# Kernel optimization log

Hardware: AMD Instinct MI355X
Metric: run time of the kernel (lower is better)

The kernel has to match this reference:

```python
import jax, jax.numpy as jnp
import numpy as np

N_NODES = 20000
N_EDGES = 640000
HIDDEN = 256
HEADS = 8
HEAD_DIM = HIDDEN // HEADS
VOCAB = 119
N_FEATS = 9


def setup_inputs() -> dict:
    key = jax.random.key(0)
    ks = jax.random.split(key, 12)
    X = jax.random.randint(ks[0], (N_NODES, N_FEATS), 0, VOCAB)
    edge_row = jnp.sort(jax.random.randint(ks[1], (N_EDGES,), 0, N_NODES))
    edge_col = jax.random.randint(ks[2], (N_EDGES,), 0, N_NODES)
    s = 0.05  # init scale to keep activations sane
    emb_tables = jax.random.normal(ks[3], (N_FEATS, VOCAB, HIDDEN), jnp.float32) * s
    q_w = jax.random.normal(ks[4], (HIDDEN, HIDDEN), jnp.float32) * s
    q_b = jax.random.normal(ks[5], (HIDDEN,), jnp.float32) * s
    k_w = jax.random.normal(ks[6], (HIDDEN, HIDDEN), jnp.float32) * s
    k_b = jax.random.normal(ks[7], (HIDDEN,), jnp.float32) * s
    v_w = jax.random.normal(ks[8], (HIDDEN, HIDDEN), jnp.float32) * s
    v_b = jax.random.normal(ks[9], (HIDDEN,), jnp.float32) * s
    o_w = jax.random.normal(ks[10], (HIDDEN, HIDDEN), jnp.float32) * s
    o_b = jax.random.normal(ks[11], (HIDDEN,), jnp.float32) * s
    return dict(X=X, edge_row=edge_row, edge_col=edge_col, emb_tables=emb_tables,
                q_w=q_w, q_b=q_b, k_w=k_w, k_b=k_b, v_w=v_w, v_b=v_b, o_w=o_w, o_b=o_b)


def reference(X, edge_row, edge_col, emb_tables, q_w, q_b, k_w, k_b, v_w, v_b, o_w, o_b):
    N = X.shape[0]
    # AtomEncoder: sum of per-feature embeddings -> [N, HIDDEN]
    feat_idx = jnp.arange(N_FEATS)[None, :]  # [1, 9]
    h = emb_tables[feat_idx, X].sum(axis=1)  # [N, 9, H] -> [N, H]
    # q/k/v projections (torch Linear: y = x W^T + b), split into heads
    q = (h @ q_w.T + q_b).reshape(N, HEADS, HEAD_DIM) * (HEAD_DIM ** -0.5)
    k = (h @ k_w.T + k_b).reshape(N, HEADS, HEAD_DIM)
    v = (h @ v_w.T + v_b).reshape(N, HEADS, HEAD_DIM)
    # SDDMM: per-edge, per-head scores
    s = jnp.einsum('ehd,ehd->eh', q[edge_row], k[edge_col])  # [E, HEADS]
    # sparse row-wise softmax (over each node's outgoing-edge neighbors)
    m = jax.ops.segment_max(s, edge_row, num_segments=N)
    e = jnp.exp(s - m[edge_row])
    z = jax.ops.segment_sum(e, edge_row, num_segments=N)
    attn = e / z[edge_row]  # [E, HEADS]
    # SPMM: weighted aggregation of neighbor values
    out = jax.ops.segment_sum(attn[:, :, None] * v[edge_col], edge_row, num_segments=N)
    return out.reshape(N, HIDDEN) @ o_w.T + o_b
```

## Files before the change

kernel.cpp:

```cpp
#include <hip/hip_runtime.h>
#include <hip/hip_bf16.h>

#define N_NODES 20000
#define N_EDGES 640000
#define HIDDEN 256
#define HEADS 8
#define HEAD_DIM 32
#define N_FEATS 9
#define VOCAB 119

typedef __hip_bfloat16 bf16;
typedef __attribute__((ext_vector_type(8))) short short8;
typedef __attribute__((ext_vector_type(4))) float f32x4;

__device__ __forceinline__ ushort f2u(float x) { union { ushort u; bf16 b; } c; c.b = __float2bfloat16(x); return c.u; }
__device__ __forceinline__ void unpack8(uint4 u, float* f) {
    f[0] = __uint_as_float(u.x << 16); f[1] = __uint_as_float(u.x & 0xffff0000u);
    f[2] = __uint_as_float(u.y << 16); f[3] = __uint_as_float(u.y & 0xffff0000u);
    f[4] = __uint_as_float(u.z << 16); f[5] = __uint_as_float(u.z & 0xffff0000u);
    f[6] = __uint_as_float(u.w << 16); f[7] = __uint_as_float(u.w & 0xffff0000u);
}
__device__ __forceinline__ uint pack2(float a, float b) {
    union { __hip_bfloat162 h; uint u; } c;
    c.h = __float22bfloat162_rn(make_float2(a, b));
    return c.u;
}

#if __has_builtin(__builtin_amdgcn_fdot2_f32_bf16)
typedef __attribute__((ext_vector_type(2))) __bf16 bf16x2_t;
__device__ __forceinline__ float dot2bf(uint a, uint b, float c) {
    return __builtin_amdgcn_fdot2_f32_bf16(__builtin_bit_cast(bf16x2_t, a),
                                           __builtin_bit_cast(bf16x2_t, b), c, false);
}
#else
__device__ __forceinline__ float dot2bf(uint a, uint b, float c) {
    return c + __uint_as_float(a << 16) * __uint_as_float(b << 16)
             + __uint_as_float(a & 0xffff0000u) * __uint_as_float(b & 0xffff0000u);
}
#endif

__global__ void k_pre(const int* __restrict__ X, const float* __restrict__ emb,
                      bf16* __restrict__ h,
                      const float* __restrict__ qw, const float* __restrict__ kw,
                      const float* __restrict__ vw, const float* __restrict__ ow,
                      const float* __restrict__ qb, const float* __restrict__ kb,
                      const float* __restrict__ vb,
                      bf16* __restrict__ wqkv, bf16* __restrict__ wo,
                      float* __restrict__ qkvb,
                      const int* __restrict__ erow, int* __restrict__ row_ptr) {
    int b = blockIdx.x;
    if (b < 5000) {
        int tid = b * 256 + threadIdx.x;
        int n = tid >> 6;
        int c4 = (tid & 63) * 4;
        float4 a = make_float4(0.f, 0.f, 0.f, 0.f);
#pragma unroll
        for (int f = 0; f < N_FEATS; ++f) {
            int idx = X[n * N_FEATS + f];
            float4 e = *(const float4*)(emb + ((size_t)(f * VOCAB + idx)) * HIDDEN + c4);
            a.x += e.x; a.y += e.y; a.z += e.z; a.w += e.w;
        }
        ushort4 o = make_ushort4(f2u(a.x), f2u(a.y), f2u(a.z), f2u(a.w));
        *(ushort4*)((ushort*)h + (size_t)n * HIDDEN + c4) = o;
    } else if (b < 6027) {
        int i = (b - 5000) * 256 + threadIdx.x;
        if (i < 196608) {
            const float* s = i < 65536 ? qw : i < 131072 ? kw : vw;
            wqkv[i] = __float2bfloat16(s[i & 65535]);
        } else if (i < 262144) {
            wo[i - 196608] = __float2bfloat16(ow[i - 196608]);
        } else if (i < 262912) {
            int j = i - 262144;
            const float* s = j < 256 ? qb : j < 512 ? kb : vb;
            qkvb[j] = s[j & 255];
        }
    } else {
        int n = (b - 6027) * 256 + threadIdx.x;
        if (n > N_NODES) return;
        int lo = 0, hi = N_EDGES;
        while (lo < hi) {
            int mid = (lo + hi) >> 1;
            if (erow[mid] < n) lo = mid + 1; else hi = mid;
        }
        row_ptr[n] = lo;
    }
}

template <int MODE, bool GUARD, int TM>
__device__ __forceinline__ void gemm_core(const bf16* __restrict__ A,
                                          const bf16* __restrict__ W,
                                          const float* __restrict__ bias,
                                          void* __restrict__ Y0, void* __restrict__ Y1,
                                          float s_q, int n0, int d0) {
    constexpr int RI = TM / 32;
    __shared__ short As[TM * 72];
    __shared__ short Bs[128 * 72];
    int t = threadIdx.x;
    int lane = t & 63, w = t >> 6;
    int wr = (w >> 1) * (TM / 2), wc = (w & 1) * 64;
    int lr = lane & 15, quad = lane >> 4;

    f32x4 acc[RI][4] = {};
    short8 ra[RI], rb[4];
    int srowA[RI], skoA[RI], srowB[4], skoB[4];
#pragma unroll
    for (int it = 0; it < RI; ++it) { int c = t + 256 * it; srowA[it] = c >> 3; skoA[it] = (c & 7) * 8; }
#pragma unroll
    for (int it = 0; it < 4; ++it) { int c = t + 256 * it; srowB[it] = c >> 3; skoB[it] = (c & 7) * 8; }

#pragma unroll
    for (int it = 0; it < RI; ++it) {
        int n = n0 + srowA[it];
        short8 av = {};
        if (!GUARD || n < N_NODES) av = *(const short8*)(A + (size_t)n * HIDDEN + skoA[it]);
        ra[it] = av;
    }
#pragma unroll
    for (int it = 0; it < 4; ++it)
        rb[it] = *(const short8*)(W + (size_t)(d0 + srowB[it]) * HIDDEN + skoB[it]);
#pragma unroll
    for (int it = 0; it < RI; ++it) *(short8*)(&As[srowA[it] * 72 + skoA[it]]) = ra[it];
#pragma unroll
    for (int it = 0; it < 4; ++it)  *(short8*)(&Bs[srowB[it] * 72 + skoB[it]]) = rb[it];
    __syncthreads();

    for (int k0 = 64; k0 < 256; k0 += 64) {
#pragma unroll
        for (int it = 0; it < RI; ++it) {
            int n = n0 + srowA[it];
            short8 av = {};
            if (!GUARD || n < N_NODES) av = *(const short8*)(A + (size_t)n * HIDDEN + k0 + skoA[it]);
            ra[it] = av;
        }
#pragma unroll
        for (int it = 0; it < 4; ++it)
            rb[it] = *(const short8*)(W + (size_t)(d0 + srowB[it]) * HIDDEN + k0 + skoB[it]);
        {
            short8 af[RI][2], bfr[4][2];
#pragma unroll
            for (int i = 0; i < RI; ++i)
#pragma unroll
                for (int kk = 0; kk < 2; ++kk)
                    af[i][kk] = *(short8*)(&As[(wr + i * 16 + lr) * 72 + kk * 32 + quad * 8]);
#pragma unroll
            for (int j = 0; j < 4; ++j)
#pragma unroll
                for (int kk = 0; kk < 2; ++kk)
                    bfr[j][kk] = *(short8*)(&Bs[(wc + j * 16 + lr) * 72 + kk * 32 + quad * 8]);
#pragma unroll
            for (int kk = 0; kk < 2; ++kk)
#pragma unroll
                for (int i = 0; i < RI; ++i)
#pragma unroll
                    for (int j = 0; j < 4; ++j)
                        acc[i][j] = __builtin_amdgcn_mfma_f32_16x16x32_bf16(
                            af[i][kk], bfr[j][kk], acc[i][j], 0, 0, 0);
        }
        __syncthreads();
#pragma unroll
        for (int it = 0; it < RI; ++it) *(short8*)(&As[srowA[it] * 72 + skoA[it]]) = ra[it];
#pragma unroll
        for (int it = 0; it < 4; ++it)  *(short8*)(&Bs[srowB[it] * 72 + skoB[it]]) = rb[it];
        __syncthreads();
    }
    {
        short8 af[RI][2], bfr[4][2];
#pragma unroll
        for (int i = 0; i < RI; ++i)
#pragma unroll
            for (int kk = 0; kk < 2; ++kk)
                af[i][kk] = *(short8*)(&As[(wr + i * 16 + lr) * 72 + kk * 32 + quad * 8]);
#pragma unroll
        for (int j = 0; j < 4; ++j)
#pragma unroll
            for (int kk = 0; kk < 2; ++kk)
                bfr[j][kk] = *(short8*)(&Bs[(wc + j * 16 + lr) * 72 + kk * 32 + quad * 8]);
#pragma unroll
        for (int kk = 0; kk < 2; ++kk)
#pragma unroll
            for (int i = 0; i < RI; ++i)
#pragma unroll
                for (int j = 0; j < 4; ++j)
                    acc[i][j] = __builtin_amdgcn_mfma_f32_16x16x32_bf16(
                        af[i][kk], bfr[j][kk], acc[i][j], 0, 0, 0);
    }

#pragma unroll
    for (int j = 0; j < 4; ++j) {
        int dbase = d0 + wc + j * 16;
        float bj = bias[dbase + lr];
        if constexpr (MODE == 0) {
            float sc = (dbase < 256) ? s_q : 1.f;
            ushort* dst; int stride;
            if (dbase < 256) {
                dst = (ushort*)Y0 + (size_t)(dbase >> 6) * N_NODES * 64 + (dbase & 63) + lr;
                stride = 64;
            } else if (dbase < 512) {
                int e = dbase - 256;
                dst = (ushort*)Y1 + (size_t)(e >> 6) * N_NODES * 128 + (e & 63) + lr;
                stride = 128;
            } else {
                int e = dbase - 512;
                dst = (ushort*)Y1 + (size_t)(e >> 6) * N_NODES * 128 + 64 + (e & 63) + lr;
                stride = 128;
            }
#pragma unroll
            for (int i = 0; i < RI; ++i)
#pragma unroll
                for (int r = 0; r < 4; ++r) {
                    int n = n0 + wr + i * 16 + quad * 4 + r;
                    if (GUARD && n >= N_NODES) continue;
                    dst[(size_t)n * stride] = f2u((acc[i][j][r] + bj) * sc);
                }
        } else {
            float* dst = (float*)Y0 + dbase + lr;
#pragma unroll
            for (int i = 0; i < RI; ++i)
#pragma unroll
                for (int r = 0; r < 4; ++r) {
                    int n = n0 + wr + i * 16 + quad * 4 + r;
                    if (GUARD && n >= N_NODES) continue;
                    dst[(size_t)n * HIDDEN] = acc[i][j][r] + bj;
                }
        }
    }
}

__global__ __launch_bounds__(256, 2) void k_gemm_qkv(
    const bf16* __restrict__ A, const bf16* __restrict__ wqkv,
    const float* __restrict__ qkvb, ushort* __restrict__ qhp,
    ushort* __restrict__ kvhp, float qscale) {
    int n0 = blockIdx.x * 128;
    if (n0 + 128 <= N_NODES)
        gemm_core<0, false, 128>(A, wqkv, qkvb, qhp, kvhp, qscale, n0, blockIdx.y * 128);
    else
        gemm_core<0, true, 128>(A, wqkv, qkvb, qhp, kvhp, qscale, n0, blockIdx.y * 128);
}

__global__ __launch_bounds__(256, 4) void k_gemm_o(
    const bf16* __restrict__ A, const bf16* __restrict__ W,
    const float* __restrict__ bias, float* __restrict__ Y) {
    int n0 = blockIdx.x * 64;
    if (n0 + 64 <= N_NODES)
        gemm_core<1, false, 64>(A, W, bias, Y, nullptr, 1.f, n0, blockIdx.y * 128);
    else
        gemm_core<1, true, 64>(A, W, bias, Y, nullptr, 1.f, n0, blockIdx.y * 128);
}

__global__ __launch_bounds__(256) void k_attn(
    const int* __restrict__ row_ptr, const int* __restrict__ col,
    const ushort* __restrict__ qhp, const ushort* __restrict__ kvhp,
    bf16* __restrict__ agg) {
    int b = blockIdx.x;
    int x = b & 7;
    int hp = x & 3;
    int wave = threadIdx.x >> 6;
    int n = (b >> 3) * 8 + (x >> 2) * 4 + wave;
    int lane = threadIdx.x & 63;
    int my = lane >> 3;
    int d8 = lane & 7;

    int start = row_ptr[n];
    int deg = row_ptr[n + 1] - start;

    ushort* orow = (ushort*)agg + (size_t)n * HIDDEN + hp * 64 + d8 * 8;
    if (deg == 0) {
        if (lane < 8) { uint4 zo = {}; *(uint4*)orow = zo; }
        return;
    }

    const ushort* qrow = qhp + ((size_t)hp * N_NODES + n) * 64;
    uint4 qu = *(const uint4*)(qrow + d8 * 8);

    const ushort* kvbase = kvhp + (size_t)hp * N_NODES * 128;
    const int* cb = col + start;

    float z = 0.f;
    float av[8] = {};

    if (deg <= 64) {
        int c_all = cb[min(lane, deg - 1)];
        int nb = (deg + 7) >> 3;

        int c0 = __shfl(c_all, my);
        int c1 = __shfl(c_all, (8 + my) & 63);
        const ushort* p0 = kvbase + (((uint)c0 << 7) + (uint)d8 * 8);
        const ushort* p1 = kvbase + (((uint)c1 << 7) + (uint)d8 * 8);
        uint4 ka  = *(const uint4*)(p0), va  = *(const uint4*)(p0 + 64);
        uint4 kb2 = *(const uint4*)(p1), vb2 = *(const uint4*)(p1 + 64);

#pragma unroll 1
        for (int it = 0; it < nb; it += 2) {
            int cn0 = __shfl(c_all, ((it + 2) * 8 + my) & 63);
            int cn1 = __shfl(c_all, ((it + 3) * 8 + my) & 63);
            const ushort* pn0 = kvbase + (((uint)cn0 << 7) + (uint)d8 * 8);
            const ushort* pn1 = kvbase + (((uint)cn1 << 7) + (uint)d8 * 8);
            uint4 kn0 = *(const uint4*)(pn0), vn0 = *(const uint4*)(pn0 + 64);
            uint4 kn1 = *(const uint4*)(pn1), vn1 = *(const uint4*)(pn1 + 64);

            {
                float sa = dot2bf(ka.x, qu.x, 0.f);
                float sb = dot2bf(ka.y, qu.y, 0.f);
                sa = dot2bf(ka.z, qu.z, sa);
                sb = dot2bf(ka.w, qu.w, sb);
                float s = sa + sb;
                s += __shfl_xor(s, 1);
                s += __shfl_xor(s, 2);
                float p = (it * 8 + my < deg) ? __expf(s) : 0.f;
                z += p;
                float vf[8];
                unpack8(va, vf);
#pragma unroll
                for (int d = 0; d < 8; ++d) av[d] += p * vf[d];
            }
            {
                float sa = dot2bf(kb2.x, qu.x, 0.f);
                float sb = dot2bf(kb2.y, qu.y, 0.f);
                sa = dot2bf(kb2.z, qu.z, sa);
                sb = dot2bf(kb2.w, qu.w, sb);
                float s = sa + sb;
                s += __shfl_xor(s, 1);
                s += __shfl_xor(s, 2);
                float p = ((it + 1) * 8 + my < deg) ? __expf(s) : 0.f;
                z += p;
                float vf[8];
                unpack8(vb2, vf);
#pragma unroll
                for (int d = 0; d < 8; ++d) av[d] += p * vf[d];
            }
            ka = kn0; va = vn0; kb2 = kn1; vb2 = vn1;
        }
    } else {
        for (int i = 0; i < deg; i += 8) {
            int idx = i + my;
            int cidx = idx < deg ? idx : deg - 1;
            int c = cb[cidx];
            const ushort* kp = kvbase + (((uint)c << 7) + (uint)d8 * 8);
            uint4 ku = *(const uint4*)(kp);
            uint4 vu = *(const uint4*)(kp + 64);
            float s = dot2bf(ku.x, qu.x, 0.f);
            s = dot2bf(ku.y, qu.y, s);
            s = dot2bf(ku.z, qu.z, s);
            s = dot2bf(ku.w, qu.w, s);
            s += __shfl_xor(s, 1);
            s += __shfl_xor(s, 2);
            float p = (idx < deg) ? __expf(s) : 0.f;
            z += p;
            float vf[8];
            unpack8(vu, vf);
#pragma unroll
            for (int d = 0; d < 8; ++d) av[d] += p * vf[d];
        }
    }

    z += __shfl_xor(z, 8); z += __shfl_xor(z, 16); z += __shfl_xor(z, 32);
#pragma unroll
    for (int d = 0; d < 8; ++d) {
        av[d] += __shfl_xor(av[d], 8);
        av[d] += __shfl_xor(av[d], 16);
        av[d] += __shfl_xor(av[d], 32);
    }

    if (lane < 8) {
        float invz = 1.f / z;
        uint4 o;
        o.x = pack2(av[0] * invz, av[1] * invz);
        o.y = pack2(av[2] * invz, av[3] * invz);
        o.z = pack2(av[4] * invz, av[5] * invz);
        o.w = pack2(av[6] * invz, av[7] * invz);
        *(uint4*)orow = o;
    }
}

extern "C" void kernel_launch(void* const* d_in, const int* in_sizes, int n_in,
                              void* d_out, int out_size, void* d_ws, size_t ws_size,
                              hipStream_t stream) {
    const int*   X    = (const int*)d_in[0];
    const int*   erow = (const int*)d_in[1];
    const int*   ecol = (const int*)d_in[2];
    const float* emb  = (const float*)d_in[3];
    const float* q_w  = (const float*)d_in[4];
    const float* q_b  = (const float*)d_in[5];
    const float* k_w  = (const float*)d_in[6];
    const float* k_b  = (const float*)d_in[7];
    const float* v_w  = (const float*)d_in[8];
    const float* v_b  = (const float*)d_in[9];
    const float* o_w  = (const float*)d_in[10];
    const float* o_b  = (const float*)d_in[11];
    float* out = (float*)d_out;

    char* ws = (char*)d_ws;
    bf16*   h    = (bf16*)(ws);
    bf16*   agg  = (bf16*)(ws);
    ushort* qhp  = (ushort*)(ws + 10240000);
    ushort* kvhp = (ushort*)(ws + 20480000);
    bf16*   wqkv = (bf16*)(ws + 40960000);
    bf16*   wo   = (bf16*)(ws + 41353216);
    float*  qkvb = (float*)(ws + 41484288);
    int* row_ptr = (int*)(ws + 41487360);

    k_pre<<<6106, 256, 0, stream>>>(X, emb, h, q_w, k_w, v_w, o_w,
                                    q_b, k_b, v_b, wqkv, wo, qkvb, erow, row_ptr);

    const float qscale = 0.17677669529663687f;
    dim3 gqkv((N_NODES + 127) / 128, 768 / 128);
    k_gemm_qkv<<<gqkv, 256, 0, stream>>>(h, wqkv, qkvb, qhp, kvhp, qscale);

    k_attn<<<N_NODES, 256, 0, stream>>>(row_ptr, ecol, qhp, kvhp, agg);

    dim3 go((N_NODES + 63) / 64, HIDDEN / 128);
    k_gemm_o<<<go, 256, 0, stream>>>(agg, wo, o_b, out);
}
```

Before: 178.2 us.

## Micro-optimize attention kernel with packed FMA, DPP reductions, exp2, reduce-scatter

Rewrites the inner edge loop of the attention kernel to use packed v_pk_fma_f32 accumulation, DPP-based xor shuffles instead of ds_bpermute for the head-dim reduction, and a raw exp2 with log2(e) folded into the q scale. The final cross-lane reduction becomes a recursive-halving reduce-scatter, so each lane ends with one output dimension and stores a single bf16 instead of one lane doing a full uint4 store. The tail iteration for odd block counts is also split out to skip wasted prefetches. This trades a simpler, fully coalesced vector store for scattered 2-byte stores and relies on inline asm and DPP semantics.

```diff
diff --git a/kernel.cpp b/kernel.cpp
--- a/kernel.cpp
+++ b/kernel.cpp
@@ -12,18 +12,33 @@
 typedef __hip_bfloat16 bf16;
 typedef __attribute__((ext_vector_type(8))) short short8;
 typedef __attribute__((ext_vector_type(4))) float f32x4;
+typedef __attribute__((ext_vector_type(2))) float f32x2;
 
 __device__ __forceinline__ ushort f2u(float x) { union { ushort u; bf16 b; } c; c.b = __float2bfloat16(x); return c.u; }
-__device__ __forceinline__ void unpack8(uint4 u, float* f) {
-    f[0] = __uint_as_float(u.x << 16); f[1] = __uint_as_float(u.x & 0xffff0000u);
-    f[2] = __uint_as_float(u.y << 16); f[3] = __uint_as_float(u.y & 0xffff0000u);
-    f[4] = __uint_as_float(u.z << 16); f[5] = __uint_as_float(u.z & 0xffff0000u);
-    f[6] = __uint_as_float(u.w << 16); f[7] = __uint_as_float(u.w & 0xffff0000u);
-}
-__device__ __forceinline__ uint pack2(float a, float b) {
-    union { __hip_bfloat162 h; uint u; } c;
-    c.h = __float22bfloat162_rn(make_float2(a, b));
-    return c.u;
+
+__device__ __forceinline__ f32x2 pk_fma(f32x2 a, f32x2 b, f32x2 c) {
+    f32x2 d;
+    asm("v_pk_fma_f32 %0, %1, %2, %3" : "=v"(d) : "v"(a), "v"(b), "v"(c));
+    return d;
+}
+__device__ __forceinline__ f32x2 pk_add(f32x2 a, f32x2 b) {
+    f32x2 d;
+    asm("v_pk_add_f32 %0, %1, %2" : "=v"(d) : "v"(a), "v"(b));
+    return d;
+}
+
+template <int CTRL>
+__device__ __forceinline__ float dpp_xor(float v) {
+    return __int_as_float(__builtin_amdgcn_update_dpp(
+        0, __float_as_int(v), CTRL, 0xf, 0xf, true));
+}
+
+__device__ __forceinline__ float fast_exp2(float x) {
+#if __has_builtin(__builtin_amdgcn_exp2f)
+    return __builtin_amdgcn_exp2f(x);
+#else
+    return exp2f(x);
+#endif
 }
 
 #if __has_builtin(__builtin_amdgcn_fdot2_f32_bf16)
@@ -263,9 +278,9 @@
     int start = row_ptr[n];
     int deg = row_ptr[n + 1] - start;
 
-    ushort* orow = (ushort*)agg + (size_t)n * HIDDEN + hp * 64 + d8 * 8;
+    ushort* orow = (ushort*)agg + (size_t)n * HIDDEN + hp * 64;
     if (deg == 0) {
-        if (lane < 8) { uint4 zo = {}; *(uint4*)orow = zo; }
+        if (lane < 8) { uint4 zo = {}; *(uint4*)(orow + lane * 8) = zo; }
         return;
     }
 
@@ -274,102 +289,99 @@
 
     const ushort* kvbase = kvhp + (size_t)hp * N_NODES * 128;
     const int* cb = col + start;
+    int degm = deg - my;
 
     float z = 0.f;
-    float av[8] = {};
+    f32x2 av0 = {0.f, 0.f}, av1 = {0.f, 0.f}, av2v = {0.f, 0.f}, av3 = {0.f, 0.f};
+
+#define ATTN_COMPUTE(K, V, IT8) do {                                                      \
+        float sa_ = dot2bf((K).x, qu.x, 0.f);                                             \
+        float sb_ = dot2bf((K).y, qu.y, 0.f);                                             \
+        sa_ = dot2bf((K).z, qu.z, sa_);                                                   \
+        sb_ = dot2bf((K).w, qu.w, sb_);                                                   \
+        float s_ = sa_ + sb_;                                                             \
+        s_ += dpp_xor<0xB1>(s_);                                                          \
+        s_ += dpp_xor<0x4E>(s_);                                                          \
+        float p_ = ((IT8) < degm) ? fast_exp2(s_) : 0.f;                                  \
+        z += p_;                                                                          \
+        f32x2 pp_; pp_.x = p_; pp_.y = p_;                                                \
+        f32x2 vf0_, vf1_, vf2_, vf3_;                                                     \
+        vf0_.x = __uint_as_float((V).x << 16); vf0_.y = __uint_as_float((V).x & 0xffff0000u); \
+        vf1_.x = __uint_as_float((V).y << 16); vf1_.y = __uint_as_float((V).y & 0xffff0000u); \
+        vf2_.x = __uint_as_float((V).z << 16); vf2_.y = __uint_as_float((V).z & 0xffff0000u); \
+        vf3_.x = __uint_as_float((V).w << 16); vf3_.y = __uint_as_float((V).w & 0xffff0000u); \
+        av0  = pk_fma(vf0_, pp_, av0);                                                    \
+        av1  = pk_fma(vf1_, pp_, av1);                                                    \
+        av2v = pk_fma(vf2_, pp_, av2v);                                                   \
+        av3  = pk_fma(vf3_, pp_, av3);                                                    \
+    } while (0)
 
     if (deg <= 64) {
         int c_all = cb[min(lane, deg - 1)];
         int nb = (deg + 7) >> 3;
+        int np = nb >> 1;
 
         int c0 = __shfl(c_all, my);
         int c1 = __shfl(c_all, (8 + my) & 63);
-        const ushort* p0 = kvbase + (((uint)c0 << 7) + (uint)d8 * 8);
-        const ushort* p1 = kvbase + (((uint)c1 << 7) + (uint)d8 * 8);
-        uint4 ka  = *(const uint4*)(p0), va  = *(const uint4*)(p0 + 64);
-        uint4 kb2 = *(const uint4*)(p1), vb2 = *(const uint4*)(p1 + 64);
+        uint o0 = ((uint)c0 << 7) + (uint)d8 * 8;
+        uint o1 = ((uint)c1 << 7) + (uint)d8 * 8;
+        uint4 ka  = *(const uint4*)(kvbase + o0), va  = *(const uint4*)(kvbase + o0 + 64);
+        uint4 kb2 = *(const uint4*)(kvbase + o1), vb2 = *(const uint4*)(kvbase + o1 + 64);
 
 #pragma unroll 1
-        for (int it = 0; it < nb; it += 2) {
-            int cn0 = __shfl(c_all, ((it + 2) * 8 + my) & 63);
-            int cn1 = __shfl(c_all, ((it + 3) * 8 + my) & 63);
-            const ushort* pn0 = kvbase + (((uint)cn0 << 7) + (uint)d8 * 8);
-            const ushort* pn1 = kvbase + (((uint)cn1 << 7) + (uint)d8 * 8);
-            uint4 kn0 = *(const uint4*)(pn0), vn0 = *(const uint4*)(pn0 + 64);
-            uint4 kn1 = *(const uint4*)(pn1), vn1 = *(const uint4*)(pn1 + 64);
-
-            {
-                float sa = dot2bf(ka.x, qu.x, 0.f);
-                float sb = dot2bf(ka.y, qu.y, 0.f);
-                sa = dot2bf(ka.z, qu.z, sa);
-                sb = dot2bf(ka.w, qu.w, sb);
-                float s = sa + sb;
-                s += __shfl_xor(s, 1);
-                s += __shfl_xor(s, 2);
-                float p = (it * 8 + my < deg) ? __expf(s) : 0.f;
-                z += p;
-                float vf[8];
-                unpack8(va, vf);
-#pragma unroll
-                for (int d = 0; d < 8; ++d) av[d] += p * vf[d];
+        for (int pit = 0; pit < np; ++pit) {
+            int it = pit * 2;
+            uint4 kn0, vn0, kn1, vn1;
+            bool pf = (pit + 1 < np) || (nb & 1);
+            if (pf) {
+                int cn0 = __shfl(c_all, ((it + 2) * 8 + my) & 63);
+                int cn1 = __shfl(c_all, ((it + 3) * 8 + my) & 63);
+                uint on0 = ((uint)cn0 << 7) + (uint)d8 * 8;
+                uint on1 = ((uint)cn1 << 7) + (uint)d8 * 8;
+                kn0 = *(const uint4*)(kvbase + on0); vn0 = *(const uint4*)(kvbase + on0 + 64);
+                kn1 = *(const uint4*)(kvbase + on1); vn1 = *(const uint4*)(kvbase + on1 + 64);
             }
-            {
-                float sa = dot2bf(kb2.x, qu.x, 0.f);
-                float sb = dot2bf(kb2.y, qu.y, 0.f);
-                sa = dot2bf(kb2.z, qu.z, sa);
-                sb = dot2bf(kb2.w, qu.w, sb);
-                float s = sa + sb;
-                s += __shfl_xor(s, 1);
-                s += __shfl_xor(s, 2);
-                float p = ((it + 1) * 8 + my < deg) ? __expf(s) : 0.f;
-                z += p;
-                float vf[8];
-                unpack8(vb2, vf);
-#pragma unroll
-                for (int d = 0; d < 8; ++d) av[d] += p * vf[d];
-            }
-            ka = kn0; va = vn0; kb2 = kn1; vb2 = vn1;
-        }
+            ATTN_COMPUTE(ka, va, it * 8);
+            ATTN_COMPUTE(kb2, vb2, it * 8 + 8);
+            if (pf) { ka = kn0; va = vn0; kb2 = kn1; vb2 = vn1; }
+        }
+        if (nb & 1)
+            ATTN_COMPUTE(ka, va, (nb - 1) * 8);
     } else {
         for (int i = 0; i < deg; i += 8) {
             int idx = i + my;
             int cidx = idx < deg ? idx : deg - 1;
             int c = cb[cidx];
-            const ushort* kp = kvbase + (((uint)c << 7) + (uint)d8 * 8);
-            uint4 ku = *(const uint4*)(kp);
-            uint4 vu = *(const uint4*)(kp + 64);
-            float s = dot2bf(ku.x, qu.x, 0.f);
-            s = dot2bf(ku.y, qu.y, s);
-            s = dot2bf(ku.z, qu.z, s);
-            s = dot2bf(ku.w, qu.w, s);
-            s += __shfl_xor(s, 1);
-            s += __shfl_xor(s, 2);
-            float p = (idx < deg) ? __expf(s) : 0.f;
-            z += p;
-            float vf[8];
-            unpack8(vu, vf);
-#pragma unroll
-            for (int d = 0; d < 8; ++d) av[d] += p * vf[d];
-        }
-    }
-
-    z += __shfl_xor(z, 8); z += __shfl_xor(z, 16); z += __shfl_xor(z, 32);
-#pragma unroll
-    for (int d = 0; d < 8; ++d) {
-        av[d] += __shfl_xor(av[d], 8);
-        av[d] += __shfl_xor(av[d], 16);
-        av[d] += __shfl_xor(av[d], 32);
-    }
-
-    if (lane < 8) {
-        float invz = 1.f / z;
-        uint4 o;
-        o.x = pack2(av[0] * invz, av[1] * invz);
-        o.y = pack2(av[2] * invz, av[3] * invz);
-        o.z = pack2(av[4] * invz, av[5] * invz);
-        o.w = pack2(av[6] * invz, av[7] * invz);
-        *(uint4*)orow = o;
-    }
+            uint off = ((uint)c << 7) + (uint)d8 * 8;
+            uint4 ku = *(const uint4*)(kvbase + off);
+            uint4 vu = *(const uint4*)(kvbase + off + 64);
+            ATTN_COMPUTE(ku, vu, i);
+        }
+    }
+#undef ATTN_COMPUTE
+
+    z += dpp_xor<0x128>(z);
+    z += __shfl_xor(z, 16);
+    z += __shfl_xor(z, 32);
+
+    bool b3 = (lane & 8) != 0, b4 = (lane & 16) != 0, b5 = (lane & 32) != 0;
+    f32x2 sd0 = b3 ? av0 : av2v;
+    f32x2 sd1 = b3 ? av1 : av3;
+    f32x2 r0, r1;
+    r0.x = dpp_xor<0x128>(sd0.x); r0.y = dpp_xor<0x128>(sd0.y);
+    r1.x = dpp_xor<0x128>(sd1.x); r1.y = dpp_xor<0x128>(sd1.y);
+    f32x2 t0 = pk_add(b3 ? av2v : av0, r0);
+    f32x2 t1 = pk_add(b3 ? av3  : av1, r1);
+    f32x2 sdu = b4 ? t0 : t1;
+    f32x2 ru; ru.x = __shfl_xor(sdu.x, 16); ru.y = __shfl_xor(sdu.y, 16);
+    f32x2 u = pk_add(b4 ? t1 : t0, ru);
+    float sw = b5 ? u.x : u.y;
+    float rw = __shfl_xor(sw, 32);
+    float w = (b5 ? u.y : u.x) + rw;
+
+    int dim = d8 * 8 + ((lane >> 3) & 1) * 4 + ((lane >> 4) & 1) * 2 + ((lane >> 5) & 1);
+    float invz = 1.f / z;
+    orow[dim] = f2u(w * invz);
 }
 
 extern "C" void kernel_launch(void* const* d_in, const int* in_sizes, int n_in,
@@ -402,7 +414,7 @@
     k_pre<<<6106, 256, 0, stream>>>(X, emb, h, q_w, k_w, v_w, o_w,
                                     q_b, k_b, v_b, wqkv, wo, qkvb, erow, row_ptr);
 
-    const float qscale = 0.17677669529663687f;
+    const float qscale = 0.25503486121587466f;
     dim3 gqkv((N_NODES + 127) / 128, 768 / 128);
     k_gemm_qkv<<<gqkv, 256, 0, stream>>>(h, wqkv, qkvb, qhp, kvhp, qscale);
 
```

Result: no change. 177.9 us (-0.2%).
